# Optimization experiments

Measured on AMD Instinct MI355X. Metric: run time of the kernel, lower is better.

The kernel has to match this reference:

```python
import jax, jax.numpy as jnp
import numpy as np

B, NC, CH, HF, WF = 2, 6, 256, 32, 88
N, CIN = 100000, 128
VOXEL_SIZE = jnp.array([0.075, 0.075, 0.2], dtype=jnp.float32)
PC_MIN = jnp.array([-54.0, -54.0, -5.0], dtype=jnp.float32)
DOWNSAMPLE = 8.0
DMIN, DMAX = 1.0, 60.0


def setup_inputs() -> dict:
    key = jax.random.key(0)
    ks = jax.random.split(key, 12)
    # voxel coords: (batch, z, y, x), batch column sorted to match the
    # original per-batch-loop concatenation order
    b = jnp.repeat(jnp.arange(B, dtype=jnp.int32), N // B)
    x = jax.random.randint(ks[0], (N,), 0, 1440, dtype=jnp.int32)
    y = jax.random.randint(ks[1], (N,), 0, 1440, dtype=jnp.int32)
    z = jax.random.randint(ks[2], (N,), 0, 40, dtype=jnp.int32)
    voxel_coords = jnp.stack([b, z, y, x], axis=1)
    voxel_features = jax.random.normal(ks[3], (N, CIN), dtype=jnp.float32)
    img_feats = jax.random.normal(ks[4], (B, NC, CH, HF, WF), dtype=jnp.float32)
    # pinhole intrinsics for a 704x256 image
    K = jnp.array([[500.0, 0.0, 352.0], [0.0, 500.0, 128.0], [0.0, 0.0, 1.0]], dtype=jnp.float32)
    intrins = K + 0.01 * jax.random.normal(ks[5], (B, NC, 3, 3), dtype=jnp.float32)
    post_rots = 0.5 * jnp.eye(3, dtype=jnp.float32) + 0.001 * jax.random.normal(ks[6], (B, NC, 3, 3), dtype=jnp.float32)
    post_trans = 0.01 * jax.random.normal(ks[7], (B, NC, 3), dtype=jnp.float32)
    # bda: near-identity 4x4
    bda = jnp.tile(jnp.eye(4, dtype=jnp.float32), (B, 1, 1))
    bda = bda.at[:, :3, :3].add(0.01 * jax.random.normal(ks[8], (B, 3, 3), dtype=jnp.float32))
    bda = bda.at[:, :3, 3].set(0.1 * jax.random.normal(ks[9], (B, 3), dtype=jnp.float32))
    # lidar->cam: standard axis permutation (x->z) so depth is positive for half the scene
    R = jnp.array([[0.0, -1.0, 0.0], [0.0, 0.0, -1.0], [1.0, 0.0, 0.0]], dtype=jnp.float32)
    l2c = jnp.tile(jnp.eye(4, dtype=jnp.float32), (B, NC, 1, 1))
    l2c = l2c.at[..., :3, :3].set(R + 0.01 * jax.random.normal(ks[10], (B, NC, 3, 3), dtype=jnp.float32))
    l2c = l2c.at[..., :3, 3].set(0.1 * jax.random.normal(ks[11], (B, NC, 3), dtype=jnp.float32))
    W = 0.02 * jax.random.normal(jax.random.fold_in(key, 99), (CIN, CH), dtype=jnp.float32)
    return dict(voxel_features=voxel_features, voxel_coords=voxel_coords, img_feats=img_feats,
                intrins=intrins, post_rots=post_rots, post_trans=post_trans, bda=bda,
                lidar2cam=l2c, W=W)


def reference(voxel_features, voxel_coords, img_feats, intrins, post_rots, post_trans, bda, lidar2cam, W):
    bidx = voxel_coords[:, 0]
    # voxel index (x,y,z) -> metric lidar coords
    p = voxel_coords[:, jnp.array([3, 2, 1])].astype(jnp.float32) * VOXEL_SIZE + PC_MIN  # [N,3]
    # undo bda augmentation: (p - t) @ inv(R).T
    binv = jnp.linalg.inv(bda[:, :3, :3])  # [B,3,3]
    pcam = jnp.einsum('nj,nij->ni', p - bda[bidx, :3, 3], binv[bidx])  # [N,3]
    # lidar2img = cam2img @ lidar2cam.T (faithful to original, incl. full 4x4 transpose)
    cam2img = jnp.tile(jnp.eye(4, dtype=intrins.dtype), (B, NC, 1, 1)).at[..., :3, :3].set(intrins)
    L = cam2img @ jnp.swapaxes(lidar2cam, -1, -2)  # [B,NC,4,4]
    Lv = L[bidx]  # [N,NC,4,4]
    pimg = jnp.einsum('nj,ncij->nci', pcam, Lv[:, :, :3, :3]) + Lv[:, :, :3, 3]  # [N,NC,3]
    pimg = jnp.concatenate([pimg[..., :2] / pimg[..., 2:3], pimg[..., 2:3]], axis=-1)
    pimg = jnp.einsum('ncj,ncij->nci', pimg, post_rots[bidx]) + post_trans[bidx]
    # gather_img_feature: round/clip + masked gather, scatter into zeros == multiply by mask
    coor = jnp.round(pimg[..., :2] / DOWNSAMPLE)
    depth = pimg[..., 2]
    mask = ((coor[..., 0] >= 0) & (coor[..., 0] < WF) & (coor[..., 1] >= 0) & (coor[..., 1] < HF)
            & (depth < DMAX) & (depth >= DMIN))  # [N,NC]
    xi = jnp.clip(coor[..., 0].astype(jnp.int32), 0, WF - 1)
    yi = jnp.clip(coor[..., 1].astype(jnp.int32), 0, HF - 1)
    cams = jnp.arange(NC)[None, :]
    g = img_feats[bidx[:, None], cams, :, yi, xi]  # [N,NC,CH]
    g = g * mask[..., None].astype(g.dtype)
    # sum over cameras, then Linear(256 -> CIN, no bias)
    img_voxel = jnp.einsum('nc,oc->no', g.sum(axis=1), W)  # [N,CIN]
    out_feats = jnp.concatenate([voxel_features, img_voxel], axis=0)  # [2N,CIN]
    out_coords = jnp.concatenate([voxel_coords, voxel_coords], axis=0)  # [2N,4]
    return out_feats, out_coords
```

## Files before the change

kernel.cpp:

```cpp
#include <hip/hip_runtime.h>
#include <math.h>

#define BB   2
#define NCAM 6
#define CH   256
#define HF   32
#define WF   88
#define NV   100000
#define CIN  128
#define VPB  16
#define SGP  (CH + 4)

typedef __attribute__((ext_vector_type(8))) short short8;
typedef __attribute__((ext_vector_type(4))) float f32x4;

static __device__ inline short f2bf(float f) {
    union { float f; unsigned u; } v; v.f = f;
    unsigned r = (v.u + 0x7fffu + ((v.u >> 16) & 1u)) >> 16;
    return (short)r;
}

__global__ void prep_params_w(const float* __restrict__ intrins,
                              const float* __restrict__ post_rots,
                              const float* __restrict__ post_trans,
                              const float* __restrict__ bda,
                              const float* __restrict__ l2c,
                              const float* __restrict__ W,
                              double* __restrict__ params,
                              short*  __restrict__ Wbf)
{
    if (blockIdx.x > 0) {
        int chunk = blockIdx.x - 1;
        int l = threadIdx.x;
        int nt = chunk >> 3, kk = chunk & 7;
        int n = nt * 16 + (l & 15);
        int k = kk * 32 + (l >> 4) * 8;
        short v[8];
        #pragma unroll
        for (int j = 0; j < 8; j++) v[j] = f2bf(W[n * CH + k + j]);
        *(short8*)(Wbf + ((size_t)chunk * 64 + l) * 8) = *(short8*)v;
        return;
    }

    int t = threadIdx.x;
    if (t >= BB * NCAM) return;
    int b = t / NCAM;

    const float* Bm = bda + b * 16;
    double a00 = Bm[0], a01 = Bm[1], a02 = Bm[2],  tx = Bm[3];
    double a10 = Bm[4], a11 = Bm[5], a12 = Bm[6],  ty = Bm[7];
    double a20 = Bm[8], a21 = Bm[9], a22 = Bm[10], tz = Bm[11];

    double det = a00*(a11*a22 - a12*a21) - a01*(a10*a22 - a12*a20) + a02*(a10*a21 - a11*a20);
    double id  = 1.0 / det;
    double inv[3][3];
    inv[0][0] =  (a11*a22 - a12*a21) * id;
    inv[0][1] = -(a01*a22 - a02*a21) * id;
    inv[0][2] =  (a01*a12 - a02*a11) * id;
    inv[1][0] = -(a10*a22 - a12*a20) * id;
    inv[1][1] =  (a00*a22 - a02*a20) * id;
    inv[1][2] = -(a00*a12 - a02*a10) * id;
    inv[2][0] =  (a10*a21 - a11*a20) * id;
    inv[2][1] = -(a00*a21 - a01*a20) * id;
    inv[2][2] =  (a00*a11 - a01*a10) * id;

    const float* In = intrins + t * 9;
    const float* Lc = l2c + t * 16;

    double M3[3][3];
    #pragma unroll
    for (int i = 0; i < 3; i++)
        #pragma unroll
        for (int j = 0; j < 3; j++)
            M3[i][j] = (double)In[i*3+0] * (double)Lc[j*4+0]
                     + (double)In[i*3+1] * (double)Lc[j*4+1]
                     + (double)In[i*3+2] * (double)Lc[j*4+2];

    double M[3][3];
    #pragma unroll
    for (int i = 0; i < 3; i++)
        #pragma unroll
        for (int j = 0; j < 3; j++)
            M[i][j] = M3[i][0]*inv[0][j] + M3[i][1]*inv[1][j] + M3[i][2]*inv[2][j];

    double* P = params + t * 24;
    #pragma unroll
    for (int i = 0; i < 3; i++)
        #pragma unroll
        for (int j = 0; j < 3; j++)
            P[i*3+j] = M[i][j];
    #pragma unroll
    for (int i = 0; i < 3; i++)
        P[9+i] = -(M[i][0]*tx + M[i][1]*ty + M[i][2]*tz);
    #pragma unroll
    for (int i = 0; i < 9; i++) P[12+i] = (double)post_rots[t*9 + i];
    #pragma unroll
    for (int i = 0; i < 3; i++) P[21+i] = (double)post_trans[t*3 + i];
}

__global__ __launch_bounds__(256) void transpose_img(const float* __restrict__ img,
                                                     unsigned short* __restrict__ imgT)
{
    __shared__ float tile[32][89];
    int bid = blockIdx.x;
    int cg  = bid & 7;
    int y   = (bid >> 3) & 31;
    int bc  = bid >> 8;
    int t   = threadIdx.x;

    const float* src = img + ((size_t)(bc * CH + cg * 32)) * (HF * WF) + y * WF;
    #pragma unroll
    for (int i = 0; i < 11; i++) {
        int lin = i * 256 + t;
        int ch  = lin / 88;
        int x   = lin - ch * 88;
        tile[ch][x] = src[(size_t)ch * (HF * WF) + x];
    }
    __syncthreads();

    unsigned short* dst = imgT + ((size_t)(bc * HF + y) * WF) * CH + cg * 32;
    #pragma unroll
    for (int j = 0; j < 6; j++) {
        int lin2 = j * 256 + t;
        if (j == 5 && t >= 128) break;
        int x  = lin2 >> 4;
        int cp = lin2 & 15;
        unsigned short lo = (unsigned short)f2bf(tile[2 * cp][x]);
        unsigned short hi = (unsigned short)f2bf(tile[2 * cp + 1][x]);
        unsigned int pk = (unsigned int)lo | ((unsigned int)hi << 16);
        *(unsigned int*)(dst + (size_t)x * CH + 2 * cp) = pk;
    }
}

template <bool TRANS>
__global__ __launch_bounds__(256) void fused_gather_mm(
    const float*  __restrict__ vf,
    const int*    __restrict__ coords,
    const void*   __restrict__ imgv,
    const double* __restrict__ params,
    const short*  __restrict__ Wbf,
    float*        __restrict__ out)
{
    const int t  = threadIdx.x;
    const int n0 = blockIdx.x * VPB;

    {
        const float4* vf4 = (const float4*)vf;
        float4*       o4  = (float4*)out;
        int base = n0 * (CIN / 4);
        o4[base + t]       = vf4[base + t];
        o4[base + 256 + t] = vf4[base + 256 + t];
    }
    if (t < VPB * 4) {
        int gi = n0 * 4 + t;
        float cv = (float)coords[gi];
        const size_t cb = (size_t)2 * NV * CIN;
        out[cb + gi]                  = cv;
        out[cb + (size_t)NV * 4 + gi] = cv;
    }

    __shared__ int   pofs[VPB][NCAM];
    __shared__ float sg[VPB][SGP];
    __shared__ __align__(16) short aFrag[8 * 64 * 8];

    if (t < VPB * NCAM) {
        int vi = t / NCAM, c = t - vi * NCAM;
        int n  = n0 + vi;
        int b  = coords[n * 4 + 0];
        int zi = coords[n * 4 + 1];
        int yi = coords[n * 4 + 2];
        int xi = coords[n * 4 + 3];
        double px = (double)xi * (double)0.075f + (-54.0);
        double py = (double)yi * (double)0.075f + (-54.0);
        double pz = (double)zi * (double)0.2f   + (-5.0);
        const double* P = params + (b * NCAM + c) * 24;
        double X = P[0]*px + P[1]*py + P[2]*pz + P[9];
        double Y = P[3]*px + P[4]*py + P[5]*pz + P[10];
        double Z = P[6]*px + P[7]*py + P[8]*pz + P[11];
        double u = X / Z;
        double v = Y / Z;
        double q0 = P[12]*u + P[13]*v + P[14]*Z + P[21];
        double q1 = P[15]*u + P[16]*v + P[17]*Z + P[22];
        double q2 = P[18]*u + P[19]*v + P[20]*Z + P[23];
        double cx = rint(q0 * 0.125);
        double cy = rint(q1 * 0.125);
        bool m = (cx >= 0.0) && (cx < (double)WF) && (cy >= 0.0) && (cy < (double)HF)
              && (q2 < 60.0) && (q2 >= 1.0);
        int o = -1;
        if (m) {
            int ix = (int)cx, iy = (int)cy;
            if (TRANS) o = ((b * NCAM + c) * HF + iy) * WF + ix;
            else       o = (b * NCAM + c) * (CH * HF * WF) + iy * WF + ix;
        }
        pofs[vi][c] = o;
    }
    __syncthreads();

    if (TRANS) {
        const unsigned short* imgT = (const unsigned short*)imgv;
        int u  = t & 127;
        int vh = t >> 7;
        #pragma unroll
        for (int s = 0; s < VPB / 2; s++) {
            int vi = vh * (VPB / 2) + s;
            float g0 = 0.0f, g1 = 0.0f;
            #pragma unroll
            for (int c = 0; c < NCAM; c++) {
                int o = pofs[vi][c];
                if (o >= 0) {
                    unsigned int pk = *(const unsigned int*)(imgT + (size_t)o * CH + 2 * u);
                    union { unsigned int u; float f; } a, b;
                    a.u = pk << 16;
                    b.u = pk & 0xffff0000u;
                    g0 += a.f;
                    g1 += b.f;
                }
            }
            *(float2*)&sg[vi][2 * u] = make_float2(g0, g1);
        }
    } else {
        const float* img = (const float*)imgv;
        #pragma unroll
        for (int vi = 0; vi < VPB; vi++) {
            float g = 0.0f;
            #pragma unroll
            for (int c = 0; c < NCAM; c++) {
                int o = pofs[vi][c];
                if (o >= 0) g += img[(size_t)o + (size_t)t * (HF * WF)];
            }
            sg[vi][t] = g;
        }
    }
    __syncthreads();

    #pragma unroll
    for (int p = 0; p < 2; p++) {
        int c2 = t + p * 256;
        int kk = c2 >> 6;
        int l  = c2 & 63;
        int m  = l & 15;
        int k  = kk * 32 + (l >> 4) * 8;
        float4 v0 = *(const float4*)&sg[m][k];
        float4 v1 = *(const float4*)&sg[m][k + 4];
        short tmp[8];
        tmp[0] = f2bf(v0.x); tmp[1] = f2bf(v0.y); tmp[2] = f2bf(v0.z); tmp[3] = f2bf(v0.w);
        tmp[4] = f2bf(v1.x); tmp[5] = f2bf(v1.y); tmp[6] = f2bf(v1.z); tmp[7] = f2bf(v1.w);
        *(short8*)(aFrag + c2 * 8) = *(short8*)tmp;
    }
    __syncthreads();

    {
        const int w    = t >> 6;
        const int lane = t & 63;
        f32x4 acc0 = {0.f, 0.f, 0.f, 0.f};
        f32x4 acc1 = {0.f, 0.f, 0.f, 0.f};
        const short8* Bf = (const short8*)Wbf;
        #pragma unroll
        for (int kk = 0; kk < 8; kk++) {
            short8 a  = *(const short8*)(aFrag + (kk * 64 + lane) * 8);
            short8 b0 = Bf[((2 * w)     * 8 + kk) * 64 + lane];
            short8 b1 = Bf[((2 * w + 1) * 8 + kk) * 64 + lane];
            acc0 = __builtin_amdgcn_mfma_f32_16x16x32_bf16(a, b0, acc0, 0, 0, 0);
            acc1 = __builtin_amdgcn_mfma_f32_16x16x32_bf16(a, b1, acc1, 0, 0, 0);
        }
        float* oiv = out + (size_t)NV * CIN;
        int col = lane & 15, rq = lane >> 4;
        #pragma unroll
        for (int r = 0; r < 4; r++) {
            int n = n0 + rq * 4 + r;
            oiv[(size_t)n * CIN + (2 * w)     * 16 + col] = acc0[r];
            oiv[(size_t)n * CIN + (2 * w + 1) * 16 + col] = acc1[r];
        }
    }
}

extern "C" void kernel_launch(void* const* d_in, const int* in_sizes, int n_in,
                              void* d_out, int out_size, void* d_ws, size_t ws_size,
                              hipStream_t stream)
{
    const float* vf      = (const float*)d_in[0];
    const int*   coords  = (const int*)d_in[1];
    const float* img     = (const float*)d_in[2];
    const float* intrins = (const float*)d_in[3];
    const float* prots   = (const float*)d_in[4];
    const float* ptrans  = (const float*)d_in[5];
    const float* bda     = (const float*)d_in[6];
    const float* l2c     = (const float*)d_in[7];
    const float* W       = (const float*)d_in[8];
    float* out = (float*)d_out;

    double* params = (double*)d_ws;
    const size_t wbf_off  = 4096;
    const size_t wbf_sz   = (size_t)8 * 8 * 64 * 8 * sizeof(short);
    const size_t imgT_off = wbf_off + wbf_sz;
    const size_t needed   = imgT_off + (size_t)BB * NCAM * HF * WF * CH * sizeof(unsigned short);

    short* Wbf = (short*)((char*)d_ws + wbf_off);

    prep_params_w<<<65, 64, 0, stream>>>(intrins, prots, ptrans, bda, l2c, W, params, Wbf);

    if (ws_size >= needed) {
        unsigned short* imgT = (unsigned short*)((char*)d_ws + imgT_off);
        transpose_img<<<BB * NCAM * HF * 8, 256, 0, stream>>>(img, imgT);
        fused_gather_mm<true><<<NV / VPB, 256, 0, stream>>>(vf, coords, imgT, params, Wbf, out);
    } else {
        fused_gather_mm<false><<<NV / VPB, 256, 0, stream>>>(vf, coords, img, params, Wbf, out);
    }
}
```

Baseline: 222.3 us.

## Gather image features directly into MFMA A-fragment layout, drop staging buffer

The gather phase now has each thread accumulate 16 channels for one voxel, in exactly the slots it owns in the bf16 MFMA A-fragment. This removes the fp32 shared staging array, one barrier and the separate convert pass. Invalid projections read pixel 0 and are multiplied by a 0/1 mask weight instead of branching, so every camera read is unconditional. Each thread now issues 16-byte vector loads, at the cost of extra memory traffic for masked-out cameras and higher register use.

```diff
diff --git a/kernel.cpp b/kernel.cpp
--- a/kernel.cpp
+++ b/kernel.cpp
@@ -9,7 +9,6 @@
 #define NV   100000
 #define CIN  128
 #define VPB  16
-#define SGP  (CH + 4)
 
 typedef __attribute__((ext_vector_type(8))) short short8;
 typedef __attribute__((ext_vector_type(4))) float f32x4;
@@ -18,6 +17,12 @@
     union { float f; unsigned u; } v; v.f = f;
     unsigned r = (v.u + 0x7fffu + ((v.u >> 16) & 1u)) >> 16;
     return (short)r;
+}
+static __device__ inline float bflo(unsigned int pk) {
+    union { unsigned int u; float f; } a; a.u = pk << 16; return a.f;
+}
+static __device__ inline float bfhi(unsigned int pk) {
+    union { unsigned int u; float f; } a; a.u = pk & 0xffff0000u; return a.f;
 }
 
 __global__ void prep_params_w(const float* __restrict__ intrins,
@@ -132,6 +137,8 @@
     }
 }
 
+struct POF { int o; float m; };
+
 template <bool TRANS>
 __global__ __launch_bounds__(256) void fused_gather_mm(
     const float*  __restrict__ vf,
@@ -159,8 +166,7 @@
         out[cb + (size_t)NV * 4 + gi] = cv;
     }
 
-    __shared__ int   pofs[VPB][NCAM];
-    __shared__ float sg[VPB][SGP];
+    __shared__ POF pof[VPB][NCAM];
     __shared__ __align__(16) short aFrag[8 * 64 * 8];
 
     if (t < VPB * NCAM) {
@@ -186,66 +192,64 @@
         double cy = rint(q1 * 0.125);
         bool m = (cx >= 0.0) && (cx < (double)WF) && (cy >= 0.0) && (cy < (double)HF)
               && (q2 < 60.0) && (q2 >= 1.0);
-        int o = -1;
+        int o = 0;
         if (m) {
             int ix = (int)cx, iy = (int)cy;
             if (TRANS) o = ((b * NCAM + c) * HF + iy) * WF + ix;
             else       o = (b * NCAM + c) * (CH * HF * WF) + iy * WF + ix;
         }
-        pofs[vi][c] = o;
+        POF p2; p2.o = o; p2.m = m ? 1.0f : 0.0f;
+        pof[vi][c] = p2;
     }
     __syncthreads();
 
-    if (TRANS) {
-        const unsigned short* imgT = (const unsigned short*)imgv;
-        int u  = t & 127;
-        int vh = t >> 7;
-        #pragma unroll
-        for (int s = 0; s < VPB / 2; s++) {
-            int vi = vh * (VPB / 2) + s;
-            float g0 = 0.0f, g1 = 0.0f;
+    {
+        const int l  = t & 63;
+        const int kk = t >> 6;
+        const int vi = l & 15;
+        const int k0 = kk * 32 + ((l >> 4) & 3) * 8;
+
+        float g[16];
+        #pragma unroll
+        for (int j = 0; j < 16; j++) g[j] = 0.0f;
+
+        if (TRANS) {
+            const unsigned short* imgT = (const unsigned short*)imgv;
             #pragma unroll
             for (int c = 0; c < NCAM; c++) {
-                int o = pofs[vi][c];
-                if (o >= 0) {
-                    unsigned int pk = *(const unsigned int*)(imgT + (size_t)o * CH + 2 * u);
-                    union { unsigned int u; float f; } a, b;
-                    a.u = pk << 16;
-                    b.u = pk & 0xffff0000u;
-                    g0 += a.f;
-                    g1 += b.f;
+                POF p2 = pof[vi][c];
+                float w = p2.m;
+                const unsigned short* px = imgT + (size_t)p2.o * CH;
+                uint4 A = *(const uint4*)(px + k0);
+                uint4 B2 = *(const uint4*)(px + k0 + 128);
+                g[0]  = fmaf(w, bflo(A.x),  g[0]);  g[1]  = fmaf(w, bfhi(A.x),  g[1]);
+                g[2]  = fmaf(w, bflo(A.y),  g[2]);  g[3]  = fmaf(w, bfhi(A.y),  g[3]);
+                g[4]  = fmaf(w, bflo(A.z),  g[4]);  g[5]  = fmaf(w, bfhi(A.z),  g[5]);
+                g[6]  = fmaf(w, bflo(A.w),  g[6]);  g[7]  = fmaf(w, bfhi(A.w),  g[7]);
+                g[8]  = fmaf(w, bflo(B2.x), g[8]);  g[9]  = fmaf(w, bfhi(B2.x), g[9]);
+                g[10] = fmaf(w, bflo(B2.y), g[10]); g[11] = fmaf(w, bfhi(B2.y), g[11]);
+                g[12] = fmaf(w, bflo(B2.z), g[12]); g[13] = fmaf(w, bfhi(B2.z), g[13]);
+                g[14] = fmaf(w, bflo(B2.w), g[14]); g[15] = fmaf(w, bfhi(B2.w), g[15]);
+            }
+        } else {
+            const float* img = (const float*)imgv;
+            #pragma unroll
+            for (int c = 0; c < NCAM; c++) {
+                POF p2 = pof[vi][c];
+                float w = p2.m;
+                #pragma unroll
+                for (int j = 0; j < 8; j++) {
+                    g[j]     = fmaf(w, img[(size_t)(k0 + j)       * (HF * WF) + p2.o], g[j]);
+                    g[8 + j] = fmaf(w, img[(size_t)(k0 + 128 + j) * (HF * WF) + p2.o], g[8 + j]);
                 }
             }
-            *(float2*)&sg[vi][2 * u] = make_float2(g0, g1);
         }
-    } else {
-        const float* img = (const float*)imgv;
-        #pragma unroll
-        for (int vi = 0; vi < VPB; vi++) {
-            float g = 0.0f;
-            #pragma unroll
-            for (int c = 0; c < NCAM; c++) {
-                int o = pofs[vi][c];
-                if (o >= 0) g += img[(size_t)o + (size_t)t * (HF * WF)];
-            }
-            sg[vi][t] = g;
-        }
-    }
-    __syncthreads();
-
-    #pragma unroll
-    for (int p = 0; p < 2; p++) {
-        int c2 = t + p * 256;
-        int kk = c2 >> 6;
-        int l  = c2 & 63;
-        int m  = l & 15;
-        int k  = kk * 32 + (l >> 4) * 8;
-        float4 v0 = *(const float4*)&sg[m][k];
-        float4 v1 = *(const float4*)&sg[m][k + 4];
-        short tmp[8];
-        tmp[0] = f2bf(v0.x); tmp[1] = f2bf(v0.y); tmp[2] = f2bf(v0.z); tmp[3] = f2bf(v0.w);
-        tmp[4] = f2bf(v1.x); tmp[5] = f2bf(v1.y); tmp[6] = f2bf(v1.z); tmp[7] = f2bf(v1.w);
-        *(short8*)(aFrag + c2 * 8) = *(short8*)tmp;
+
+        short tmp[16];
+        #pragma unroll
+        for (int j = 0; j < 16; j++) tmp[j] = f2bf(g[j]);
+        *(short8*)(aFrag + (kk * 64 + l) * 8)       = *(short8*)&tmp[0];
+        *(short8*)(aFrag + ((kk + 4) * 64 + l) * 8) = *(short8*)&tmp[8];
     }
     __syncthreads();
 
```

Result: no change. 222.1 us (-0.1%).
